# Optimization experiments

Measured on AMD Instinct MI355X. Metric: run time of the kernel, lower is better.

The kernel has to match this reference:

```python
import jax, jax.numpy as jnp
import numpy as np
import math

M = 0.5
S = 64.0
TH = math.cos(math.pi - M)           # threshold cos(pi - m)
MM = math.sin(math.pi - M) * M       # sin(pi - m) * m
EPS = 1e-12

def _l2norm(x, axis=-1):
    return x / jnp.sqrt(jnp.sum(x * x, axis=axis, keepdims=True) + EPS)

def setup_inputs() -> dict:
    key = jax.random.key(0)
    k1, k2, k3 = jax.random.split(key, 3)
    B, D, C = 512, 512, 100000
    features = jax.random.normal(k1, (B, D), dtype=jnp.float32)
    weight = jax.random.normal(k2, (C, D), dtype=jnp.float32)
    labels = jax.random.randint(k3, (B,), 0, C, dtype=jnp.int32)
    return {"features": features, "labels": labels, "weight": weight}

def reference(features, labels, weight):
    # cos_theta: [B, C] = normalized features @ normalized weight^T
    cos_theta = jnp.einsum('bd,cd->bc', _l2norm(features), _l2norm(weight))
    cos_theta = jnp.clip(cos_theta, -1.0, 1.0)
    B = features.shape[0]
    rows = jnp.arange(B)
    # margin correction only affects the target column per row; gather it
    tgt_cos = cos_theta[rows, labels]                      # [B]
    theta_m = jnp.arccos(tgt_cos) + M
    cos_theta_m = jnp.cos(theta_m)
    tgt_adj = jnp.where(tgt_cos > TH, cos_theta_m, tgt_cos - MM)
    output = cos_theta.at[rows, labels].set(tgt_adj)
    return S * output
```

## Files before the change

kernel.cpp:

```cpp
#include <hip/hip_runtime.h>


typedef __attribute__((ext_vector_type(8))) short short8;
typedef __attribute__((ext_vector_type(8))) unsigned short u16x8;
typedef __attribute__((ext_vector_type(4))) float f32x4;

#define TH_CONST  (-0.8775825618903728f)
#define MM_CONST  (0.23971276930210156f)
#define M_MARGIN  0.5f
#define S_SCALE   64.0f
#define KD 512

__device__ __forceinline__ unsigned short f2bf(float x) {
    unsigned int u = __float_as_uint(x);
    u += 0x7fffu + ((u >> 16) & 1u);
    return (unsigned short)(u >> 16);
}

__global__ __launch_bounds__(256)
void convert_norm_kernel(const float* __restrict__ W,
                         const float* __restrict__ F,
                         unsigned short* __restrict__ Wb,
                         unsigned short* __restrict__ Fb,
                         float* __restrict__ invW,
                         float* __restrict__ invF,
                         const int C, const int B)
{
    const int lane = threadIdx.x & 63;
    int gw = blockIdx.x * 4 + (threadIdx.x >> 6);
    const int stride = gridDim.x * 4;
    const int total = C + B;

    for (int row = gw; row < total; row += stride) {
        const float* src;
        unsigned short* dst;
        float* inv;
        if (row < C) {
            src = W + (size_t)row * KD;
            dst = Wb + (size_t)row * KD;
            inv = invW + row;
        } else {
            const int r = row - C;
            src = F + (size_t)r * KD;
            dst = Fb + (size_t)r * KD;
            inv = invF + r;
        }
        const float4* p = (const float4*)(src + lane * 8);
        float4 v0 = p[0], v1 = p[1];

        float ss = v0.x*v0.x + v0.y*v0.y + v0.z*v0.z + v0.w*v0.w
                 + v1.x*v1.x + v1.y*v1.y + v1.z*v1.z + v1.w*v1.w;

        u16x8 pk;
        pk[0]=f2bf(v0.x); pk[1]=f2bf(v0.y); pk[2]=f2bf(v0.z); pk[3]=f2bf(v0.w);
        pk[4]=f2bf(v1.x); pk[5]=f2bf(v1.y); pk[6]=f2bf(v1.z); pk[7]=f2bf(v1.w);
        *(u16x8*)(dst + lane * 8) = pk;

        ss += __shfl_xor(ss, 1);
        ss += __shfl_xor(ss, 2);
        ss += __shfl_xor(ss, 4);
        ss += __shfl_xor(ss, 8);
        ss += __shfl_xor(ss, 16);
        ss += __shfl_xor(ss, 32);
        if (lane == 0) *inv = 1.0f / sqrtf(ss + 1e-12f);
    }
}

__device__ __forceinline__ void gload_lds_16(const void* g, void* l) {
    __builtin_amdgcn_global_load_lds(
        (const __attribute__((address_space(1))) unsigned int*)g,
        (__attribute__((address_space(3))) unsigned int*)l,
        16, 0, 0);
}

__global__ __launch_bounds__(256, 2)
void arcface_gemm_kernel(const unsigned short* __restrict__ Fb,
                         const unsigned short* __restrict__ Wb,
                         const float* __restrict__ invF,
                         const float* __restrict__ invW,
                         const int*   __restrict__ labels,
                         float*       __restrict__ Out,
                         const int C, const int GM)
{
    __shared__ unsigned short As[128 * 32];
    __shared__ unsigned short Bs[128 * 32];
    __shared__ float nF[128];
    __shared__ float nW[128];
    __shared__ int   Ls[128];

    const int nwg = gridDim.x;
    const int bid = blockIdx.x;
    const int q   = nwg >> 3, rr = nwg & 7;
    const int xcd = bid & 7,  seq = bid >> 3;
    const int wg  = (xcd < rr ? xcd * (q + 1) : rr * (q + 1) + (xcd - rr) * q) + seq;
    const int mt  = wg % GM;
    const int nt  = wg / GM;

    const int m_base = mt * 128;
    const int n_base = nt * 128;

    const int t    = threadIdx.x;
    const int wave = t >> 6;
    const int lane = t & 63;
    const int wm   = (wave >> 1) * 64;
    const int wn   = (wave & 1) * 64;
    const int quad = lane >> 4;
    const int lcol = lane & 15;

    if (t < 128) {
        nF[t] = invF[m_base + t];
        const int c = n_base + t;
        nW[t] = (c < C) ? invW[c] : 0.f;
        Ls[t] = labels[m_base + t];
    }

    const int off0 = t * 16;
    const int ar0  = off0 >> 6;
    const int cb0  = off0 & 63;
    const int ar1  = ar0 + 64;

    const char* gA0 = (const char*)Fb + (size_t)(m_base + ar0) * (KD * 2) + cb0;
    const char* gA1 = (const char*)Fb + (size_t)(m_base + ar1) * (KD * 2) + cb0;
    int b0 = n_base + ar0; if (b0 >= C) b0 = C - 1;
    int b1 = n_base + ar1; if (b1 >= C) b1 = C - 1;
    const char* gB0 = (const char*)Wb + (size_t)b0 * (KD * 2) + cb0;
    const char* gB1 = (const char*)Wb + (size_t)b1 * (KD * 2) + cb0;

    char* lA0 = (char*)As + wave * 1024;
    char* lA1 = (char*)As + 4096 + wave * 1024;
    char* lB0 = (char*)Bs + wave * 1024;
    char* lB1 = (char*)Bs + 4096 + wave * 1024;

    f32x4 acc[4][4];
    #pragma unroll
    for (int i = 0; i < 4; ++i)
        #pragma unroll
        for (int j = 0; j < 4; ++j)
            acc[i][j] = (f32x4){0.f, 0.f, 0.f, 0.f};

    #pragma unroll 1
    for (int kt = 0; kt < KD / 32; ++kt) {
        gload_lds_16(gA0 + kt * 64, lA0);
        gload_lds_16(gA1 + kt * 64, lA1);
        gload_lds_16(gB0 + kt * 64, lB0);
        gload_lds_16(gB1 + kt * 64, lB1);
        __syncthreads();

        short8 af[4], bfr[4];
        #pragma unroll
        for (int i = 0; i < 4; ++i) {
            af[i]  = *(const short8*)&As[(wm + i * 16 + lcol) * 32 + quad * 8];
            bfr[i] = *(const short8*)&Bs[(wn + i * 16 + lcol) * 32 + quad * 8];
        }
        #pragma unroll
        for (int i = 0; i < 4; ++i)
            #pragma unroll
            for (int j = 0; j < 4; ++j)
                acc[i][j] = __builtin_amdgcn_mfma_f32_16x16x32_bf16(
                                af[i], bfr[j], acc[i][j], 0, 0, 0);
        __syncthreads();
    }

    #pragma unroll
    for (int mi = 0; mi < 4; ++mi) {
        const int rl_base = wm + mi * 16 + quad * 4;
        #pragma unroll
        for (int rg = 0; rg < 4; ++rg) {
            const int rl = rl_base + rg;
            const float invf = nF[rl];
            const int lbl = Ls[rl];
            float* orow = Out + (size_t)(m_base + rl) * C;
            #pragma unroll
            for (int ni = 0; ni < 4; ++ni) {
                const int cl = wn + ni * 16 + lcol;
                const int gcol = n_base + cl;
                if (gcol < C) {
                    float v = acc[mi][ni][rg] * invf * nW[cl];
                    v = fminf(1.0f, fmaxf(-1.0f, v));
                    if (gcol == lbl) {
                        v = (v > TH_CONST) ? cosf(acosf(v) + M_MARGIN)
                                           : (v - MM_CONST);
                    }
                    orow[gcol] = S_SCALE * v;
                }
            }
        }
    }
}

#define BM 128
#define BN 128
#define BK 32

__global__ __launch_bounds__(256, 2)
void arcface_fused_kernel(const float* __restrict__ F,
                          const int*   __restrict__ labels,
                          const float* __restrict__ W,
                          float*       __restrict__ Out,
                          const int C)
{
    __shared__ unsigned short As[BM][BK];
    __shared__ unsigned short Bs[BN][BK];
    __shared__ float normF[BM];
    __shared__ float normW[BN];
    __shared__ int   Ls[BM];

    const int t = threadIdx.x;
    const int m_base = blockIdx.x * BM;
    const int n_base = blockIdx.y * BN;

    if (t < BM) Ls[t] = labels[m_base + t];

    const int r = t >> 1;
    const int h = t & 1;

    const int lane = t & 63;
    const int wave = t >> 6;
    const int wm = (wave >> 1) * 64;
    const int wn = (wave & 1) * 64;
    const int quad = lane >> 4;
    const int lcol = lane & 15;

    f32x4 acc[4][4];
    #pragma unroll
    for (int i = 0; i < 4; ++i)
        #pragma unroll
        for (int j = 0; j < 4; ++j)
            acc[i][j] = (f32x4){0.f, 0.f, 0.f, 0.f};

    const int cls = n_base + r;
    const bool cvalid = (cls < C);

    const float* Arow = F + (size_t)(m_base + r) * KD + h * 16;
    const float* Wrow = W + (size_t)(cvalid ? cls : 0) * KD + h * 16;

    float sF = 0.f, sW = 0.f;

    for (int kt = 0; kt < KD / BK; ++kt) {
        const float4* ap = (const float4*)(Arow + kt * BK);
        const float4* wp = (const float4*)(Wrow + kt * BK);
        float4 a0 = ap[0], a1 = ap[1], a2 = ap[2], a3 = ap[3];
        float4 w0, w1, w2, w3;
        if (cvalid) { w0 = wp[0]; w1 = wp[1]; w2 = wp[2]; w3 = wp[3]; }
        else { w0 = make_float4(0.f,0.f,0.f,0.f); w1 = w0; w2 = w0; w3 = w0; }

        sF += a0.x*a0.x + a0.y*a0.y + a0.z*a0.z + a0.w*a0.w
            + a1.x*a1.x + a1.y*a1.y + a1.z*a1.z + a1.w*a1.w
            + a2.x*a2.x + a2.y*a2.y + a2.z*a2.z + a2.w*a2.w
            + a3.x*a3.x + a3.y*a3.y + a3.z*a3.z + a3.w*a3.w;
        sW += w0.x*w0.x + w0.y*w0.y + w0.z*w0.z + w0.w*w0.w
            + w1.x*w1.x + w1.y*w1.y + w1.z*w1.z + w1.w*w1.w
            + w2.x*w2.x + w2.y*w2.y + w2.z*w2.z + w2.w*w2.w
            + w3.x*w3.x + w3.y*w3.y + w3.z*w3.z + w3.w*w3.w;

        u16x8 pa0, pa1, pb0, pb1;
        pa0[0]=f2bf(a0.x); pa0[1]=f2bf(a0.y); pa0[2]=f2bf(a0.z); pa0[3]=f2bf(a0.w);
        pa0[4]=f2bf(a1.x); pa0[5]=f2bf(a1.y); pa0[6]=f2bf(a1.z); pa0[7]=f2bf(a1.w);
        pa1[0]=f2bf(a2.x); pa1[1]=f2bf(a2.y); pa1[2]=f2bf(a2.z); pa1[3]=f2bf(a2.w);
        pa1[4]=f2bf(a3.x); pa1[5]=f2bf(a3.y); pa1[6]=f2bf(a3.z); pa1[7]=f2bf(a3.w);
        pb0[0]=f2bf(w0.x); pb0[1]=f2bf(w0.y); pb0[2]=f2bf(w0.z); pb0[3]=f2bf(w0.w);
        pb0[4]=f2bf(w1.x); pb0[5]=f2bf(w1.y); pb0[6]=f2bf(w1.z); pb0[7]=f2bf(w1.w);
        pb1[0]=f2bf(w2.x); pb1[1]=f2bf(w2.y); pb1[2]=f2bf(w2.z); pb1[3]=f2bf(w2.w);
        pb1[4]=f2bf(w3.x); pb1[5]=f2bf(w3.y); pb1[6]=f2bf(w3.z); pb1[7]=f2bf(w3.w);

        __syncthreads();
        *((u16x8*)&As[r][h*16])     = pa0;
        *((u16x8*)&As[r][h*16 + 8]) = pa1;
        *((u16x8*)&Bs[r][h*16])     = pb0;
        *((u16x8*)&Bs[r][h*16 + 8]) = pb1;
        __syncthreads();

        short8 af[4], bfr[4];
        #pragma unroll
        for (int i = 0; i < 4; ++i) {
            af[i]  = *(const short8*)&As[wm + i*16 + lcol][quad*8];
            bfr[i] = *(const short8*)&Bs[wn + i*16 + lcol][quad*8];
        }
        #pragma unroll
        for (int i = 0; i < 4; ++i)
            #pragma unroll
            for (int j = 0; j < 4; ++j)
                acc[i][j] = __builtin_amdgcn_mfma_f32_16x16x32_bf16(
                                af[i], bfr[j], acc[i][j], 0, 0, 0);
    }

    sF += __shfl_xor(sF, 1);
    sW += __shfl_xor(sW, 1);
    if (h == 0) {
        normF[r] = 1.0f / sqrtf(sF + 1e-12f);
        normW[r] = 1.0f / sqrtf(sW + 1e-12f);
    }
    __syncthreads();

    #pragma unroll
    for (int mi = 0; mi < 4; ++mi) {
        const int rl_base = wm + mi*16 + quad*4;
        #pragma unroll
        for (int rg = 0; rg < 4; ++rg) {
            const int rl = rl_base + rg;
            const float invf = normF[rl];
            const int lbl = Ls[rl];
            float* orow = Out + (size_t)(m_base + rl) * C;
            #pragma unroll
            for (int ni = 0; ni < 4; ++ni) {
                const int cl = wn + ni*16 + lcol;
                const int gcol = n_base + cl;
                if (gcol < C) {
                    float v = acc[mi][ni][rg] * invf * normW[cl];
                    v = fminf(1.0f, fmaxf(-1.0f, v));
                    if (gcol == lbl) {
                        v = (v > TH_CONST) ? cosf(acosf(v) + M_MARGIN)
                                           : (v - MM_CONST);
                    }
                    orow[gcol] = S_SCALE * v;
                }
            }
        }
    }
}

extern "C" void kernel_launch(void* const* d_in, const int* in_sizes, int n_in,
                              void* d_out, int out_size, void* d_ws, size_t ws_size,
                              hipStream_t stream) {
    const float* F      = (const float*)d_in[0];
    const int*   labels = (const int*)d_in[1];
    const float* W      = (const float*)d_in[2];
    float*       Out    = (float*)d_out;

    const int B = in_sizes[1];
    const int C = in_sizes[2] / KD;

    const size_t a = 255;
    size_t offWb = 0;
    size_t szWb  = (size_t)C * KD * sizeof(unsigned short);
    size_t offFb = (offWb + szWb + a) & ~a;
    size_t szFb  = (size_t)B * KD * sizeof(unsigned short);
    size_t offIW = (offFb + szFb + a) & ~a;
    size_t szIW  = (size_t)C * sizeof(float);
    size_t offIF = (offIW + szIW + a) & ~a;
    size_t szIF  = (size_t)B * sizeof(float);
    size_t need  = offIF + szIF;

    if (d_ws != nullptr && ws_size >= need && (B % 128) == 0) {
        unsigned short* Wb   = (unsigned short*)((char*)d_ws + offWb);
        unsigned short* Fb   = (unsigned short*)((char*)d_ws + offFb);
        float*          invW = (float*)((char*)d_ws + offIW);
        float*          invF = (float*)((char*)d_ws + offIF);

        convert_norm_kernel<<<2048, 256, 0, stream>>>(W, F, Wb, Fb, invW, invF, C, B);

        const int GM = B / 128;
        const int NT = (C + 127) / 128;
        arcface_gemm_kernel<<<GM * NT, 256, 0, stream>>>(Fb, Wb, invF, invW,
                                                         labels, Out, C, GM);
    } else {
        dim3 grid(B / BM, (C + BN - 1) / BN);
        arcface_fused_kernel<<<grid, dim3(256), 0, stream>>>(F, labels, W, Out, C);
    }
}
```

Baseline: 462.9 us.

## Deepen GEMM K-tile to 64 with XOR-swizzled LDS and nontemporal output stores

The GEMM kernel now loads 64-wide K slices per iteration instead of 32. This halves the number of barrier pairs, and an XOR swizzle on the LDS column offset is meant to avoid bank conflicts. The launch bound is raised to 4 blocks per CU, output stores become nontemporal to avoid cache pollution, and the convert kernel handles two rows per wave with 32 lanes each. The larger LDS footprint (32KB) and the higher occupancy target may raise register pressure or cause spills.

```diff
diff --git a/kernel.cpp b/kernel.cpp
--- a/kernel.cpp
+++ b/kernel.cpp
@@ -27,42 +27,56 @@
                          const int C, const int B)
 {
     const int lane = threadIdx.x & 63;
-    int gw = blockIdx.x * 4 + (threadIdx.x >> 6);
+    const int half = lane >> 5;
+    const int l5   = lane & 31;
+    const int total  = C + B;
+    const int npairs = (total + 1) >> 1;
+
+    int pair = blockIdx.x * 4 + (threadIdx.x >> 6);
     const int stride = gridDim.x * 4;
-    const int total = C + B;
-
-    for (int row = gw; row < total; row += stride) {
-        const float* src;
-        unsigned short* dst;
-        float* inv;
-        if (row < C) {
-            src = W + (size_t)row * KD;
-            dst = Wb + (size_t)row * KD;
-            inv = invW + row;
-        } else {
-            const int r = row - C;
-            src = F + (size_t)r * KD;
-            dst = Fb + (size_t)r * KD;
-            inv = invF + r;
-        }
-        const float4* p = (const float4*)(src + lane * 8);
-        float4 v0 = p[0], v1 = p[1];
-
-        float ss = v0.x*v0.x + v0.y*v0.y + v0.z*v0.z + v0.w*v0.w
-                 + v1.x*v1.x + v1.y*v1.y + v1.z*v1.z + v1.w*v1.w;
-
-        u16x8 pk;
-        pk[0]=f2bf(v0.x); pk[1]=f2bf(v0.y); pk[2]=f2bf(v0.z); pk[3]=f2bf(v0.w);
-        pk[4]=f2bf(v1.x); pk[5]=f2bf(v1.y); pk[6]=f2bf(v1.z); pk[7]=f2bf(v1.w);
-        *(u16x8*)(dst + lane * 8) = pk;
+
+    for (; pair < npairs; pair += stride) {
+        const int row = pair * 2 + half;
+        const bool valid = (row < total);
+        float ss = 0.f;
+        float* inv = nullptr;
+        unsigned short* dst = nullptr;
+
+        if (valid) {
+            const float* src;
+            if (row < C) {
+                src = W + (size_t)row * KD;
+                dst = Wb + (size_t)row * KD;
+                inv = invW + row;
+            } else {
+                const int r = row - C;
+                src = F + (size_t)r * KD;
+                dst = Fb + (size_t)r * KD;
+                inv = invF + r;
+            }
+            const float4* p = (const float4*)(src + l5 * 16);
+            float4 v0 = p[0], v1 = p[1], v2 = p[2], v3 = p[3];
+
+            ss = v0.x*v0.x + v0.y*v0.y + v0.z*v0.z + v0.w*v0.w
+               + v1.x*v1.x + v1.y*v1.y + v1.z*v1.z + v1.w*v1.w
+               + v2.x*v2.x + v2.y*v2.y + v2.z*v2.z + v2.w*v2.w
+               + v3.x*v3.x + v3.y*v3.y + v3.z*v3.z + v3.w*v3.w;
+
+            u16x8 pk0, pk1;
+            pk0[0]=f2bf(v0.x); pk0[1]=f2bf(v0.y); pk0[2]=f2bf(v0.z); pk0[3]=f2bf(v0.w);
+            pk0[4]=f2bf(v1.x); pk0[5]=f2bf(v1.y); pk0[6]=f2bf(v1.z); pk0[7]=f2bf(v1.w);
+            pk1[0]=f2bf(v2.x); pk1[1]=f2bf(v2.y); pk1[2]=f2bf(v2.z); pk1[3]=f2bf(v2.w);
+            pk1[4]=f2bf(v3.x); pk1[5]=f2bf(v3.y); pk1[6]=f2bf(v3.z); pk1[7]=f2bf(v3.w);
+            *(u16x8*)(dst + l5 * 16)     = pk0;
+            *(u16x8*)(dst + l5 * 16 + 8) = pk1;
+        }
 
         ss += __shfl_xor(ss, 1);
         ss += __shfl_xor(ss, 2);
         ss += __shfl_xor(ss, 4);
         ss += __shfl_xor(ss, 8);
         ss += __shfl_xor(ss, 16);
-        ss += __shfl_xor(ss, 32);
-        if (lane == 0) *inv = 1.0f / sqrtf(ss + 1e-12f);
+        if (valid && l5 == 0) *inv = 1.0f / sqrtf(ss + 1e-12f);
     }
 }
 
@@ -73,7 +87,7 @@
         16, 0, 0);
 }
 
-__global__ __launch_bounds__(256, 2)
+__global__ __launch_bounds__(256, 4)
 void arcface_gemm_kernel(const unsigned short* __restrict__ Fb,
                          const unsigned short* __restrict__ Wb,
                          const float* __restrict__ invF,
@@ -82,8 +96,8 @@
                          float*       __restrict__ Out,
                          const int C, const int GM)
 {
-    __shared__ unsigned short As[128 * 32];
-    __shared__ unsigned short Bs[128 * 32];
+    __shared__ unsigned short As[128 * 64];
+    __shared__ unsigned short Bs[128 * 64];
     __shared__ float nF[128];
     __shared__ float nW[128];
     __shared__ int   Ls[128];
@@ -114,22 +128,22 @@
         Ls[t] = labels[m_base + t];
     }
 
-    const int off0 = t * 16;
-    const int ar0  = off0 >> 6;
-    const int cb0  = off0 & 63;
-    const int ar1  = ar0 + 64;
-
-    const char* gA0 = (const char*)Fb + (size_t)(m_base + ar0) * (KD * 2) + cb0;
-    const char* gA1 = (const char*)Fb + (size_t)(m_base + ar1) * (KD * 2) + cb0;
-    int b0 = n_base + ar0; if (b0 >= C) b0 = C - 1;
-    int b1 = n_base + ar1; if (b1 >= C) b1 = C - 1;
-    const char* gB0 = (const char*)Wb + (size_t)b0 * (KD * 2) + cb0;
-    const char* gB1 = (const char*)Wb + (size_t)b1 * (KD * 2) + cb0;
-
-    char* lA0 = (char*)As + wave * 1024;
-    char* lA1 = (char*)As + 4096 + wave * 1024;
-    char* lB0 = (char*)Bs + wave * 1024;
-    char* lB1 = (char*)Bs + 4096 + wave * 1024;
+    const int rbase  = t >> 3;
+    const int colSwz = (((t & 7) ^ ((t >> 3) & 7)) << 4);
+
+    const char* gA = (const char*)Fb + (size_t)(m_base + rbase) * (KD * 2) + colSwz;
+
+    unsigned int offB[4];
+    #pragma unroll
+    for (int c = 0; c < 4; ++c) {
+        int rb = n_base + c * 32 + rbase;
+        if (rb >= C) rb = C - 1;
+        offB[c] = (unsigned int)rb * (KD * 2) + colSwz;
+    }
+    const char* gWb = (const char*)Wb;
+
+    char* lA = (char*)As + wave * 1024;
+    char* lB = (char*)Bs + wave * 1024;
 
     f32x4 acc[4][4];
     #pragma unroll
@@ -138,19 +152,41 @@
         for (int j = 0; j < 4; ++j)
             acc[i][j] = (f32x4){0.f, 0.f, 0.f, 0.f};
 
+    const int sw = (lcol & 7) << 4;
+
     #pragma unroll 1
-    for (int kt = 0; kt < KD / 32; ++kt) {
-        gload_lds_16(gA0 + kt * 64, lA0);
-        gload_lds_16(gA1 + kt * 64, lA1);
-        gload_lds_16(gB0 + kt * 64, lB0);
-        gload_lds_16(gB1 + kt * 64, lB1);
+    for (int kt = 0; kt < KD / 64; ++kt) {
+        const int ko = kt * 128;
+        #pragma unroll
+        for (int c = 0; c < 4; ++c)
+            gload_lds_16(gA + c * 32768 + ko, lA + c * 4096);
+        #pragma unroll
+        for (int c = 0; c < 4; ++c)
+            gload_lds_16(gWb + offB[c] + ko, lB + c * 4096);
         __syncthreads();
 
         short8 af[4], bfr[4];
         #pragma unroll
         for (int i = 0; i < 4; ++i) {
-            af[i]  = *(const short8*)&As[(wm + i * 16 + lcol) * 32 + quad * 8];
-            bfr[i] = *(const short8*)&Bs[(wn + i * 16 + lcol) * 32 + quad * 8];
+            const int ra = (wm + i * 16 + lcol) * 128;
+            const int rb = (wn + i * 16 + lcol) * 128;
+            const int co = (quad * 16) ^ sw;
+            af[i]  = *(const short8*)((const char*)As + ra + co);
+            bfr[i] = *(const short8*)((const char*)Bs + rb + co);
+        }
+        #pragma unroll
+        for (int i = 0; i < 4; ++i)
+            #pragma unroll
+            for (int j = 0; j < 4; ++j)
+                acc[i][j] = __builtin_amdgcn_mfma_f32_16x16x32_bf16(
+                                af[i], bfr[j], acc[i][j], 0, 0, 0);
+        #pragma unroll
+        for (int i = 0; i < 4; ++i) {
+            const int ra = (wm + i * 16 + lcol) * 128;
+            const int rb = (wn + i * 16 + lcol) * 128;
+            const int co = (64 | (quad * 16)) ^ sw;
+            af[i]  = *(const short8*)((const char*)As + ra + co);
+            bfr[i] = *(const short8*)((const char*)Bs + rb + co);
         }
         #pragma unroll
         for (int i = 0; i < 4; ++i)
@@ -181,7 +217,7 @@
                         v = (v > TH_CONST) ? cosf(acosf(v) + M_MARGIN)
                                            : (v - MM_CONST);
                     }
-                    orow[gcol] = S_SCALE * v;
+                    __builtin_nontemporal_store(S_SCALE * v, &orow[gcol]);
                 }
             }
         }
@@ -199,17 +235,17 @@
                           float*       __restrict__ Out,
                           const int C)
 {
-    __shared__ unsigned short As[BM][BK];
-    __shared__ unsigned short Bs[BN][BK];
+    __shared__ unsigned short Asf[BM][BK];
+    __shared__ unsigned short Bsf[BN][BK];
     __shared__ float normF[BM];
     __shared__ float normW[BN];
-    __shared__ int   Ls[BM];
+    __shared__ int   Lsf[BM];
 
     const int t = threadIdx.x;
     const int m_base = blockIdx.x * BM;
     const int n_base = blockIdx.y * BN;
 
-    if (t < BM) Ls[t] = labels[m_base + t];
+    if (t < BM) Lsf[t] = labels[m_base + t];
 
     const int r = t >> 1;
     const int h = t & 1;
@@ -264,17 +300,17 @@
         pb1[4]=f2bf(w3.x); pb1[5]=f2bf(w3.y); pb1[6]=f2bf(w3.z); pb1[7]=f2bf(w3.w);
 
         __syncthreads();
-        *((u16x8*)&As[r][h*16])     = pa0;
-        *((u16x8*)&As[r][h*16 + 8]) = pa1;
-        *((u16x8*)&Bs[r][h*16])     = pb0;
-        *((u16x8*)&Bs[r][h*16 + 8]) = pb1;
+        *((u16x8*)&Asf[r][h*16])     = pa0;
+        *((u16x8*)&Asf[r][h*16 + 8]) = pa1;
+        *((u16x8*)&Bsf[r][h*16])     = pb0;
+        *((u16x8*)&Bsf[r][h*16 + 8]) = pb1;
         __syncthreads();
 
         short8 af[4], bfr[4];
         #pragma unroll
         for (int i = 0; i < 4; ++i) {
-            af[i]  = *(const short8*)&As[wm + i*16 + lcol][quad*8];
-            bfr[i] = *(const short8*)&Bs[wn + i*16 + lcol][quad*8];
+            af[i]  = *(const short8*)&Asf[wm + i*16 + lcol][quad*8];
+            bfr[i] = *(const short8*)&Bsf[wn + i*16 + lcol][quad*8];
         }
         #pragma unroll
         for (int i = 0; i < 4; ++i)
@@ -299,7 +335,7 @@
         for (int rg = 0; rg < 4; ++rg) {
             const int rl = rl_base + rg;
             const float invf = normF[rl];
-            const int lbl = Ls[rl];
+            const int lbl = Lsf[rl];
             float* orow = Out + (size_t)(m_base + rl) * C;
             #pragma unroll
             for (int ni = 0; ni < 4; ++ni) {
```

Result: faster. 448.8 us (-3.0%).
